# Optimization experiments

Measured on AMD Instinct MI355X. Metric: run time of the kernel, lower is better.

## Reference

```python
import jax, jax.numpy as jnp
import numpy as np

B, S, T, C, Q = 8, 4096, 2048, 256, 256  # batch, ctx_steps, q_steps, context_size, query_size


def setup_inputs() -> dict:
    key = jax.random.key(0)
    k1, k2, k3, k4 = jax.random.split(key, 4)
    context = jax.random.normal(k1, (B, S, C), dtype=jnp.float32)
    query = jax.random.normal(k2, (T, B, Q), dtype=jnp.float32)
    context_mask = jax.random.randint(k3, (B, S), 0, 2).astype(bool)  # True = masked
    W = jax.random.normal(k4, (C, Q), dtype=jnp.float32)  # bilinear weights [context_size, query_size]
    return {"context": context, "query": query, "context_mask": context_mask, "W": W}


def reference(context, query, context_mask, W):
    # temp = 'auto' -> sqrt(query_size)
    temp = jnp.asarray(np.sqrt(Q), dtype=context.dtype)
    # scores[b,t,s] = (context[b,s,:] @ W) . query[t,b,:]
    scores = jnp.einsum('bsc,cq,tbq->bts', context, W, query) / temp
    neg = jnp.finfo(scores.dtype).min
    scores = jnp.where(context_mask[:, None, :], neg, scores)  # mask over ctx_steps
    attn = jax.nn.softmax(scores, axis=2)  # [B, T, S]
    # rows whose entire context is masked -> attention zeroed
    all_masked = jnp.all(context_mask, axis=1)[:, None, None]
    attn = jnp.where(all_masked, jnp.zeros((), attn.dtype), attn)
    composition = jnp.einsum('bts,bsc->btc', attn, context)  # [B, T, C]
    # module returns (attn, composition) permuted to [T, B, ...]
    return attn.transpose(1, 0, 2), composition.transpose(1, 0, 2)
```

## Files before the change

### kernel.cpp

```cpp
#include <hip/hip_runtime.h>

#define B_ 8
#define S_ 4096
#define T_ 2048
#define C_ 256
#define Q_ 256
#define NROW (T_ * B_)

typedef _Float16 f16;
typedef _Float16 f16x8 __attribute__((ext_vector_type(8)));
typedef _Float16 f16x4 __attribute__((ext_vector_type(4)));
typedef float f32x4 __attribute__((ext_vector_type(4)));

#define MFMA(a, b, c) __builtin_amdgcn_mfma_f32_16x16x32_f16((a), (b), (c), 0, 0, 0)

__global__ void k_mask_mode(const unsigned char* __restrict__ mb, int* __restrict__ mode,
                            int* __restrict__ allm) {
  __shared__ int s0_, s123_;
  if (threadIdx.x == 0) { s0_ = 0; s123_ = 0; }
  __syncthreads();
  int a0 = 0, a123 = 0;
  int base = threadIdx.x * 128;
  for (int i = 0; i < 128; ++i) {
    int idx = base + i;
    int v = mb[idx];
    if (idx & 3) a123 |= v; else a0 |= v;
  }
  if (a0) atomicOr(&s0_, 1);
  if (a123) atomicOr(&s123_, 1);
  __syncthreads();
  if (threadIdx.x == 0) {
    int m;
    if (s123_ == 0 && s0_ == 0) m = 3;
    else if (s123_ == 0) m = 0;
    else if (s0_ == 0) m = 2;
    else m = 1;
    *mode = m;
  }
  if (threadIdx.x < B_) allm[threadIdx.x] = 1;
}

__global__ void k_expand_mask(const void* __restrict__ mp, const int* __restrict__ mode,
                              float* __restrict__ maskf, int* __restrict__ allm) {
  int i = blockIdx.x * 256 + threadIdx.x;
  int md = *mode;
  int m;
  if (md == 0)      m = ((const int*)mp)[i] != 0;
  else if (md == 1) m = ((const unsigned char*)mp)[i] != 0;
  else if (md == 2) m = ((const float*)mp)[i] != 0.0f;
  else              m = 0;
  maskf[i] = m ? 1.0f : 0.0f;
  if (!m) atomicAnd(&allm[i / S_], 0);
}

__global__ void k_conv_w(const float* __restrict__ W, f16* __restrict__ WT) {
  int i = blockIdx.x * 256 + threadIdx.x;
  int c = i >> 8, q = i & 255;
  WT[q * C_ + c] = (f16)W[i];
}

__global__ void k_conv_q(const float* __restrict__ q, f16* __restrict__ qT) {
  int i = blockIdx.x * 256 + threadIdx.x;
  int e = i * 4;
  int t = e / (B_ * Q_);
  int rb = e - t * (B_ * Q_);
  int b = rb >> 8;
  int qq = rb & 255;
  f32x4 v = *(const f32x4*)(q + e);
  f16x4 h; h[0] = (f16)v[0]; h[1] = (f16)v[1]; h[2] = (f16)v[2]; h[3] = (f16)v[3];
  *(f16x4*)(qT + ((size_t)(b * T_ + t)) * Q_ + qq) = h;
}

__global__ void k_transpose_ctx(const float* __restrict__ ctx, f16* __restrict__ ctxT) {
  __shared__ f16 tile[64][65];
  int s0 = blockIdx.x * 64, c0 = blockIdx.y * 64, b = blockIdx.z;
  int r = threadIdx.x >> 2;
  int cs = (threadIdx.x & 3) * 16;
  const float* src = ctx + ((size_t)(b * S_ + s0 + r)) * C_ + c0 + cs;
  f32x4 v0 = ((const f32x4*)src)[0];
  f32x4 v1 = ((const f32x4*)src)[1];
  f32x4 v2 = ((const f32x4*)src)[2];
  f32x4 v3 = ((const f32x4*)src)[3];
#pragma unroll
  for (int j = 0; j < 4; ++j) {
    tile[r][cs + j] = (f16)v0[j];
    tile[r][cs + 4 + j] = (f16)v1[j];
    tile[r][cs + 8 + j] = (f16)v2[j];
    tile[r][cs + 12 + j] = (f16)v3[j];
  }
  __syncthreads();
  int c = threadIdx.x >> 2;
  int ss = (threadIdx.x & 3) * 16;
  f16x8 o0, o1;
#pragma unroll
  for (int j = 0; j < 8; ++j) { o0[j] = tile[ss + j][c]; o1[j] = tile[ss + 8 + j][c]; }
  f16* dst = ctxT + ((size_t)(b * C_ + c0 + c)) * S_ + s0 + ss;
  *(f16x8*)dst = o0;
  *(f16x8*)(dst + 8) = o1;
}

__launch_bounds__(256, 2)
__global__ void k_gemm_cw(const float* __restrict__ ctx, const f16* __restrict__ WT,
                          f16* __restrict__ CW) {
  __shared__ alignas(16) f16 As[128 * 32];
  __shared__ alignas(16) f16 Bs[128 * 32];
  int n0 = blockIdx.x * 128;
  int m0 = blockIdx.y * 128;
  int tid = threadIdx.x;
  int w = tid >> 6, l = tid & 63;
  int wm = (w >> 1) * 64, wn = (w & 1) * 64;
  int lr = l & 15, lk = (l >> 4) * 8;
  f32x4 acc[4][4] = {};
  for (int k0 = 0; k0 < C_; k0 += 32) {
    __syncthreads();
#pragma unroll
    for (int it = 0; it < 2; ++it) {
      int h = (it * 256 + tid) * 8;
      int row = h >> 5, kk = h & 31;
      const float* ap = ctx + (size_t)(m0 + row) * C_ + k0 + kk;
      f32x4 x0 = ((const f32x4*)ap)[0];
      f32x4 x1 = ((const f32x4*)ap)[1];
      f16x8 hv;
#pragma unroll
      for (int j = 0; j < 4; ++j) { hv[j] = (f16)x0[j]; hv[4 + j] = (f16)x1[j]; }
      *(f16x8*)&As[row * 32 + kk] = hv;
    }
#pragma unroll
    for (int it = 0; it < 2; ++it) {
      int h = (it * 256 + tid) * 8;
      int row = h >> 5, kk = h & 31;
      *(f16x8*)&Bs[row * 32 + kk] = *(const f16x8*)&WT[(size_t)(n0 + row) * C_ + k0 + kk];
    }
    __syncthreads();
    f16x8 af[4], bf[4];
#pragma unroll
    for (int m = 0; m < 4; ++m) af[m] = *(const f16x8*)&As[(wm + m * 16 + lr) * 32 + lk];
#pragma unroll
    for (int n = 0; n < 4; ++n) bf[n] = *(const f16x8*)&Bs[(wn + n * 16 + lr) * 32 + lk];
#pragma unroll
    for (int m = 0; m < 4; ++m)
#pragma unroll
      for (int n = 0; n < 4; ++n) acc[m][n] = MFMA(af[m], bf[n], acc[m][n]);
  }
#pragma unroll
  for (int m = 0; m < 4; ++m)
#pragma unroll
    for (int n = 0; n < 4; ++n)
#pragma unroll
      for (int i = 0; i < 4; ++i) {
        int gm = m0 + wm + m * 16 + (l >> 4) * 4 + i;
        int gn = n0 + wn + n * 16 + lr;
        CW[(size_t)gm * Q_ + gn] = (f16)(acc[m][n][i] * 0.0625f);
      }
}

__launch_bounds__(256, 2)
__global__ void k_gemm_scores(const f16* __restrict__ qT, const f16* __restrict__ CW,
                              const float* __restrict__ maskf, float* __restrict__ attn,
                              float* __restrict__ pmax, float* __restrict__ psum) {
  __shared__ alignas(16) f16 As[128 * 32];
  __shared__ alignas(16) f16 Bs[128 * 32];
  int n0 = blockIdx.x * 128;
  int m0 = blockIdx.y * 128;
  int b = blockIdx.z;
  const f16* A = qT + (size_t)b * T_ * Q_;
  const f16* Bm = CW + (size_t)b * S_ * Q_;
  int tid = threadIdx.x;
  int w = tid >> 6, l = tid & 63;
  int wm = (w >> 1) * 64, wn = (w & 1) * 64;
  int lr = l & 15, lk = (l >> 4) * 8;
  f32x4 acc[4][4] = {};
  for (int k0 = 0; k0 < Q_; k0 += 32) {
    __syncthreads();
#pragma unroll
    for (int it = 0; it < 2; ++it) {
      int h = (it * 256 + tid) * 8;
      int row = h >> 5, kk = h & 31;
      *(f16x8*)&As[row * 32 + kk] = *(const f16x8*)&A[(size_t)(m0 + row) * Q_ + k0 + kk];
    }
#pragma unroll
    for (int it = 0; it < 2; ++it) {
      int h = (it * 256 + tid) * 8;
      int row = h >> 5, kk = h & 31;
      *(f16x8*)&Bs[row * 32 + kk] = *(const f16x8*)&Bm[(size_t)(n0 + row) * Q_ + k0 + kk];
    }
    __syncthreads();
    f16x8 af[4], bf[4];
#pragma unroll
    for (int m = 0; m < 4; ++m) af[m] = *(const f16x8*)&As[(wm + m * 16 + lr) * 32 + lk];
#pragma unroll
    for (int n = 0; n < 4; ++n) bf[n] = *(const f16x8*)&Bs[(wn + n * 16 + lr) * 32 + lk];
#pragma unroll
    for (int m = 0; m < 4; ++m)
#pragma unroll
      for (int n = 0; n < 4; ++n) acc[m][n] = MFMA(af[m], bf[n], acc[m][n]);
  }
  float msk[4];
#pragma unroll
  for (int n = 0; n < 4; ++n) msk[n] = maskf[b * S_ + n0 + wn + n * 16 + lr];
#pragma unroll
  for (int m = 0; m < 4; ++m)
#pragma unroll
    for (int n = 0; n < 4; ++n) {
      int gn = n0 + wn + n * 16 + lr;
#pragma unroll
      for (int i = 0; i < 4; ++i) {
        int gt = m0 + wm + m * 16 + (l >> 4) * 4 + i;
        float v = acc[m][n][i];
        if (msk[n] != 0.0f) v = -3.4e38f;
        acc[m][n][i] = v;
        attn[((size_t)gt * B_ + b) * S_ + gn] = v;
      }
    }
  int g = l >> 4;
  int ch = blockIdx.x * 2 + (w & 1);
#pragma unroll
  for (int m = 0; m < 4; ++m)
#pragma unroll
    for (int i = 0; i < 4; ++i) {
      float mx = fmaxf(fmaxf(acc[m][0][i], acc[m][1][i]), fmaxf(acc[m][2][i], acc[m][3][i]));
      mx = fmaxf(mx, __shfl_xor(mx, 1));
      mx = fmaxf(mx, __shfl_xor(mx, 2));
      mx = fmaxf(mx, __shfl_xor(mx, 4));
      mx = fmaxf(mx, __shfl_xor(mx, 8));
      float sm = 0.0f;
#pragma unroll
      for (int n = 0; n < 4; ++n) sm += __expf(acc[m][n][i] - mx);
      sm += __shfl_xor(sm, 1);
      sm += __shfl_xor(sm, 2);
      sm += __shfl_xor(sm, 4);
      sm += __shfl_xor(sm, 8);
      if (lr == 0) {
        int gt = m0 + wm + m * 16 + g * 4 + i;
        int r = gt * B_ + b;
        pmax[ch * NROW + r] = mx;
        psum[ch * NROW + r] = sm;
      }
    }
}

__global__ void k_finalize(const float* __restrict__ pmax, const float* __restrict__ psum,
                           float* __restrict__ rmax, float* __restrict__ rsum) {
  int r = blockIdx.x * 256 + threadIdx.x;
  float mx = -3.4e38f;
#pragma unroll 8
  for (int c = 0; c < 64; ++c) mx = fmaxf(mx, pmax[c * NROW + r]);
  float s = 0.0f;
#pragma unroll 8
  for (int c = 0; c < 64; ++c) s += psum[c * NROW + r] * __expf(pmax[c * NROW + r] - mx);
  rmax[r] = mx;
  rsum[r] = s;
}

__launch_bounds__(256, 2)
__global__ void k_comp(float* __restrict__ attn, const f16* __restrict__ ctxT,
                       const float* __restrict__ rmax, const float* __restrict__ rsum,
                       const int* __restrict__ allm, float* __restrict__ comp) {
  __shared__ alignas(16) f16 As[2][32 * 64];
  __shared__ alignas(16) f16 Bs[2][256 * 64];
  const int t0 = blockIdx.x * 32;
  const int b = blockIdx.y;
  const int tid = threadIdx.x;
  const int w = tid >> 6, l = tid & 63;
  const int lr = l & 15, hi = l >> 4;
  const int am = allm[b];
  const int ar = tid >> 4;
  const int cg = tid & 15;
  float mx0, mx1, inv0, inv1;
  float* aP0;
  float* aP1;
  {
    int r0 = (t0 + ar) * B_ + b;
    int r1 = (t0 + 16 + ar) * B_ + b;
    mx0 = rmax[r0]; mx1 = rmax[r1];
    inv0 = am ? 0.0f : (1.0f / rsum[r0]);
    inv1 = am ? 0.0f : (1.0f / rsum[r1]);
    aP0 = attn + (size_t)r0 * S_ + cg * 4;
    aP1 = attn + (size_t)r1 * S_ + cg * 4;
  }
  const int aswz = (cg * 8) ^ ((ar & 7) << 4);
  const int bc = tid >> 3;
  const int bs = tid & 7;
  const f16* bP = ctxT + ((size_t)(b * C_ + bc)) * S_ + bs * 8;
  const int bswz = (bs * 16) ^ ((bc & 7) << 4);
  f32x4 acc[2][4] = {};
  f32x4 aC0 = *(const f32x4*)aP0;
  f32x4 aC1 = *(const f32x4*)aP1;
  f16x8 bC[8];
#pragma unroll
  for (int i = 0; i < 8; ++i) bC[i] = *(const f16x8*)(bP + (size_t)i * 32 * S_);
  for (int k = 0; k < S_ / 64; ++k) {
    const int cur = k & 1;
    const int kn = (k + 1) * 64;
    f32x4 aN0 = *(const f32x4*)(aP0 + kn);
    f32x4 aN1 = *(const f32x4*)(aP1 + kn);
    f16x8 bN[8];
#pragma unroll
    for (int i = 0; i < 8; ++i) bN[i] = *(const f16x8*)(bP + (size_t)i * 32 * S_ + kn);
    f32x4 p0, p1;
#pragma unroll
    for (int e = 0; e < 4; ++e) {
      p0[e] = __expf(aC0[e] - mx0) * inv0;
      p1[e] = __expf(aC1[e] - mx1) * inv1;
    }
    *(f32x4*)(aP0 + k * 64) = p0;
    *(f32x4*)(aP1 + k * 64) = p1;
    f16x4 h0, h1;
#pragma unroll
    for (int e = 0; e < 4; ++e) { h0[e] = (f16)p0[e]; h1[e] = (f16)p1[e]; }
    *(f16x4*)((char*)As[cur] + ar * 128 + aswz) = h0;
    *(f16x4*)((char*)As[cur] + (16 + ar) * 128 + aswz) = h1;
#pragma unroll
    for (int i = 0; i < 8; ++i)
      *(f16x8*)((char*)Bs[cur] + (i * 32 + bc) * 128 + bswz) = bC[i];
    asm volatile("s_waitcnt lgkmcnt(0)" ::: "memory");
    __builtin_amdgcn_s_barrier();
    __builtin_amdgcn_sched_barrier(0);
#pragma unroll
    for (int kk = 0; kk < 2; ++kk) {
      const int cb = (kk * 64 + hi * 16) ^ ((lr & 7) << 4);
      f16x8 af[2], bf[4];
#pragma unroll
      for (int m = 0; m < 2; ++m)
        af[m] = *(const f16x8*)((char*)As[cur] + (m * 16 + lr) * 128 + cb);
#pragma unroll
      for (int n = 0; n < 4; ++n)
        bf[n] = *(const f16x8*)((char*)Bs[cur] + (w * 64 + n * 16 + lr) * 128 + cb);
#pragma unroll
      for (int m = 0; m < 2; ++m)
#pragma unroll
        for (int n = 0; n < 4; ++n) acc[m][n] = MFMA(af[m], bf[n], acc[m][n]);
    }
    aC0 = aN0; aC1 = aN1;
#pragma unroll
    for (int i = 0; i < 8; ++i) bC[i] = bN[i];
  }
#pragma unroll
  for (int m = 0; m < 2; ++m)
#pragma unroll
    for (int n = 0; n < 4; ++n)
#pragma unroll
      for (int i = 0; i < 4; ++i) {
        int tl = m * 16 + hi * 4 + i;
        int cc = w * 64 + n * 16 + lr;
        comp[((size_t)(t0 + tl) * B_ + b) * C_ + cc] = acc[m][n][i];
      }
}

extern "C" void kernel_launch(void* const* d_in, const int* in_sizes, int n_in,
                              void* d_out, int out_size, void* d_ws, size_t ws_size,
                              hipStream_t stream) {
  const float* ctx = (const float*)d_in[0];
  const float* query = (const float*)d_in[1];
  const void* mask = d_in[2];
  const float* W = (const float*)d_in[3];

  float* out = (float*)d_out;
  float* attn = out;
  float* comp = out + (size_t)T_ * B_ * S_;
  f16* CW = (f16*)comp;

  char* ws = (char*)d_ws;
  f16* ctxT = (f16*)(ws);
  f16* qT = (f16*)(ws + 16777216);
  f16* WT = (f16*)(ws + 25165824);
  float* maskf = (float*)(ws + 25296896);
  float* rmax = (float*)(ws + 25427968);
  float* rsum = (float*)(ws + 25493504);
  int* allm = (int*)(ws + 25559040);
  int* mode = (int*)(ws + 25559072);
  float* pmax = (float*)(ws + 25559168);
  float* psum = (float*)(ws + 29753472);

  k_mask_mode<<<1, 256, 0, stream>>>((const unsigned char*)mask, mode, allm);
  k_expand_mask<<<(B_ * S_) / 256, 256, 0, stream>>>(mask, mode, maskf, allm);
  k_conv_w<<<(C_ * Q_) / 256, 256, 0, stream>>>(W, WT);
  k_conv_q<<<(T_ * B_ * Q_ / 4) / 256, 256, 0, stream>>>(query, qT);
  k_transpose_ctx<<<dim3(S_ / 64, C_ / 64, B_), 256, 0, stream>>>(ctx, ctxT);
  k_gemm_cw<<<dim3(Q_ / 128, (B_ * S_) / 128), 256, 0, stream>>>(ctx, WT, CW);
  k_gemm_scores<<<dim3(S_ / 128, T_ / 128, B_), 256, 0, stream>>>(qT, CW, maskf, attn, pmax, psum);
  k_finalize<<<NROW / 256, 256, 0, stream>>>(pmax, psum, rmax, rsum);
  k_comp<<<dim3(T_ / 32, B_), 256, 0, stream>>>(attn, ctxT, rmax, rsum, allm, comp);
}
```

Before: 554.9 us.

## Recompute scores in fused softmax-composition kernel instead of round-tripping attn

Splits the scores pass into a stats-only GEMM that writes no attention matrix, then a fused kernel that recomputes scores per 64-column tile, normalizes with the final row max and sum, writes attn once, and feeds the fp16 probabilities straight from shared memory into the composition MFMA. This removes the first full write of the 268MB fp32 attn tensor and the k_comp pass that reads it back, at the cost of doing the QK GEMM twice. CW moves to a separate workspace region so comp is not aliased, and the old path is kept as a fallback when the workspace is too small.

Result: slower. 568.7 us (+2.5%).

```diff
diff --git a/kernel.cpp b/kernel.cpp
--- a/kernel.cpp
+++ b/kernel.cpp
@@ -210,6 +210,86 @@
         if (msk[n] != 0.0f) v = -3.4e38f;
         acc[m][n][i] = v;
         attn[((size_t)gt * B_ + b) * S_ + gn] = v;
+      }
+    }
+  int g = l >> 4;
+  int ch = blockIdx.x * 2 + (w & 1);
+#pragma unroll
+  for (int m = 0; m < 4; ++m)
+#pragma unroll
+    for (int i = 0; i < 4; ++i) {
+      float mx = fmaxf(fmaxf(acc[m][0][i], acc[m][1][i]), fmaxf(acc[m][2][i], acc[m][3][i]));
+      mx = fmaxf(mx, __shfl_xor(mx, 1));
+      mx = fmaxf(mx, __shfl_xor(mx, 2));
+      mx = fmaxf(mx, __shfl_xor(mx, 4));
+      mx = fmaxf(mx, __shfl_xor(mx, 8));
+      float sm = 0.0f;
+#pragma unroll
+      for (int n = 0; n < 4; ++n) sm += __expf(acc[m][n][i] - mx);
+      sm += __shfl_xor(sm, 1);
+      sm += __shfl_xor(sm, 2);
+      sm += __shfl_xor(sm, 4);
+      sm += __shfl_xor(sm, 8);
+      if (lr == 0) {
+        int gt = m0 + wm + m * 16 + g * 4 + i;
+        int r = gt * B_ + b;
+        pmax[ch * NROW + r] = mx;
+        psum[ch * NROW + r] = sm;
+      }
+    }
+}
+
+__launch_bounds__(256, 2)
+__global__ void k_gemm_stats(const f16* __restrict__ qT, const f16* __restrict__ CW,
+                             const float* __restrict__ maskf,
+                             float* __restrict__ pmax, float* __restrict__ psum) {
+  __shared__ alignas(16) f16 As[128 * 32];
+  __shared__ alignas(16) f16 Bs[128 * 32];
+  int n0 = blockIdx.x * 128;
+  int m0 = blockIdx.y * 128;
+  int b = blockIdx.z;
+  const f16* A = qT + (size_t)b * T_ * Q_;
+  const f16* Bm = CW + (size_t)b * S_ * Q_;
+  int tid = threadIdx.x;
+  int w = tid >> 6, l = tid & 63;
+  int wm = (w >> 1) * 64, wn = (w & 1) * 64;
+  int lr = l & 15, lk = (l >> 4) * 8;
+  f32x4 acc[4][4] = {};
+  for (int k0 = 0; k0 < Q_; k0 += 32) {
+    __syncthreads();
+#pragma unroll
+    for (int it = 0; it < 2; ++it) {
+      int h = (it * 256 + tid) * 8;
+      int row = h >> 5, kk = h & 31;
+      *(f16x8*)&As[row * 32 + kk] = *(const f16x8*)&A[(size_t)(m0 + row) * Q_ + k0 + kk];
+    }
+#pragma unroll
+    for (int it = 0; it < 2; ++it) {
+      int h = (it * 256 + tid) * 8;
+      int row = h >> 5, kk = h & 31;
+      *(f16x8*)&Bs[row * 32 + kk] = *(const f16x8*)&Bm[(size_t)(n0 + row) * Q_ + k0 + kk];
+    }
+    __syncthreads();
+    f16x8 af[4], bf[4];
+#pragma unroll
+    for (int m = 0; m < 4; ++m) af[m] = *(const f16x8*)&As[(wm + m * 16 + lr) * 32 + lk];
+#pragma unroll
+    for (int n = 0; n < 4; ++n) bf[n] = *(const f16x8*)&Bs[(wn + n * 16 + lr) * 32 + lk];
+#pragma unroll
+    for (int m = 0; m < 4; ++m)
+#pragma unroll
+      for (int n = 0; n < 4; ++n) acc[m][n] = MFMA(af[m], bf[n], acc[m][n]);
+  }
+  float msk[4];
+#pragma unroll
+  for (int n = 0; n < 4; ++n) msk[n] = maskf[b * S_ + n0 + wn + n * 16 + lr];
+#pragma unroll
+  for (int m = 0; m < 4; ++m)
+#pragma unroll
+    for (int n = 0; n < 4; ++n) {
+      if (msk[n] != 0.0f) {
+#pragma unroll
+        for (int i = 0; i < 4; ++i) acc[m][n][i] = -3.4e38f;
       }
     }
   int g = l >> 4;
@@ -347,6 +427,110 @@
       }
 }
 
+__launch_bounds__(256, 2)
+__global__ void k_fused(const f16* __restrict__ qT, const f16* __restrict__ CW,
+                        const f16* __restrict__ ctxT, const float* __restrict__ maskf,
+                        const float* __restrict__ rmax, const float* __restrict__ rsum,
+                        const int* __restrict__ allm,
+                        float* __restrict__ attn, float* __restrict__ comp) {
+  __shared__ alignas(16) f16 Bs[64 * 256];
+  __shared__ alignas(16) f16 Ps[32 * 64];
+  const int bid = blockIdx.x;
+  const int b = bid & 7, tc = bid >> 3;
+  const int t0 = tc * 32;
+  const int tid = threadIdx.x;
+  const int w = tid >> 6, l = tid & 63;
+  const int lr = l & 15, hi = l >> 4;
+  const int rswz = (lr & 7) << 4;
+  const int am = allm[b];
+  float smax[2][4], sinv[2][4];
+#pragma unroll
+  for (int m = 0; m < 2; ++m)
+#pragma unroll
+    for (int i = 0; i < 4; ++i) {
+      int r = (t0 + m * 16 + hi * 4 + i) * B_ + b;
+      smax[m][i] = rmax[r];
+      sinv[m][i] = am ? 0.0f : (1.0f / rsum[r]);
+    }
+  f16x8 af[2][8];
+#pragma unroll
+  for (int m = 0; m < 2; ++m)
+#pragma unroll
+    for (int kq = 0; kq < 8; ++kq)
+      af[m][kq] = *(const f16x8*)(qT + ((size_t)(b * T_ + t0 + m * 16 + lr)) * Q_ + kq * 32 + hi * 8);
+  const int brow = tid & 63;
+  const int bcolB = (tid >> 6) * 128;
+  const int bswz = (brow & 7) << 4;
+  const f16* cwBase = CW + (size_t)b * S_ * Q_;
+  {
+    const f16* src = cwBase + (size_t)brow * Q_ + bcolB / 2;
+#pragma unroll
+    for (int j = 0; j < 8; ++j)
+      *(f16x8*)((char*)Bs + ((brow * 512 + bcolB + j * 16) ^ bswz)) = *(const f16x8*)(src + j * 8);
+  }
+  float mk = maskf[b * S_ + w * 16 + lr];
+  f32x4 accC[2][4] = {};
+  __syncthreads();
+  for (int k = 0; k < S_ / 64; ++k) {
+    const int s0 = k * 64;
+    f32x4 accS[2] = {};
+#pragma unroll
+    for (int kq = 0; kq < 8; ++kq) {
+      f16x8 bfr = *(const f16x8*)((char*)Bs + (((w * 16 + lr) * 512 + kq * 64 + hi * 16) ^ rswz));
+#pragma unroll
+      for (int m = 0; m < 2; ++m) accS[m] = MFMA(af[m][kq], bfr, accS[m]);
+    }
+#pragma unroll
+    for (int m = 0; m < 2; ++m)
+#pragma unroll
+      for (int i = 0; i < 4; ++i) {
+        int tl = m * 16 + hi * 4 + i;
+        float p = (mk != 0.0f) ? 0.0f : __expf(accS[m][i] - smax[m][i]) * sinv[m][i];
+        attn[((size_t)(t0 + tl) * B_ + b) * S_ + s0 + w * 16 + lr] = p;
+        *(f16*)((char*)Ps + ((tl * 128 + (w * 16 + lr) * 2) ^ ((tl & 7) << 4))) = (f16)p;
+      }
+    __syncthreads();
+    f16x8 gB[8];
+    if (k < S_ / 64 - 1) {
+      const f16* src = cwBase + (size_t)(s0 + 64 + brow) * Q_ + bcolB / 2;
+#pragma unroll
+      for (int j = 0; j < 8; ++j) gB[j] = *(const f16x8*)(src + j * 8);
+    }
+    float mkn = (k < S_ / 64 - 1) ? maskf[b * S_ + s0 + 64 + w * 16 + lr] : 0.0f;
+#pragma unroll
+    for (int kk = 0; kk < 2; ++kk) {
+      f16x8 pa[2];
+#pragma unroll
+      for (int m = 0; m < 2; ++m)
+        pa[m] = *(const f16x8*)((char*)Ps + (((m * 16 + lr) * 128 + kk * 64 + hi * 16) ^ rswz));
+#pragma unroll
+      for (int n = 0; n < 4; ++n) {
+        f16x8 bc = *(const f16x8*)(ctxT + ((size_t)(b * C_ + w * 64 + n * 16 + lr)) * S_
+                                   + s0 + kk * 32 + hi * 8);
+#pragma unroll
+        for (int m = 0; m < 2; ++m) accC[m][n] = MFMA(pa[m], bc, accC[m][n]);
+      }
+    }
+    if (k < S_ / 64 - 1) {
+#pragma unroll
+      for (int j = 0; j < 8; ++j)
+        *(f16x8*)((char*)Bs + ((brow * 512 + bcolB + j * 16) ^ bswz)) = gB[j];
+    }
+    mk = mkn;
+    __syncthreads();
+  }
+#pragma unroll
+  for (int m = 0; m < 2; ++m)
+#pragma unroll
+    for (int n = 0; n < 4; ++n)
+#pragma unroll
+      for (int i = 0; i < 4; ++i) {
+        int tl = m * 16 + hi * 4 + i;
+        int cc = w * 64 + n * 16 + lr;
+        comp[((size_t)(t0 + tl) * B_ + b) * C_ + cc] = accC[m][n][i];
+      }
+}
+
 extern "C" void kernel_launch(void* const* d_in, const int* in_sizes, int n_in,
                               void* d_out, int out_size, void* d_ws, size_t ws_size,
                               hipStream_t stream) {
@@ -358,7 +542,6 @@
   float* out = (float*)d_out;
   float* attn = out;
   float* comp = out + (size_t)T_ * B_ * S_;
-  f16* CW = (f16*)comp;
 
   char* ws = (char*)d_ws;
   f16* ctxT = (f16*)(ws);
@@ -377,8 +560,19 @@
   k_conv_w<<<(C_ * Q_) / 256, 256, 0, stream>>>(W, WT);
   k_conv_q<<<(T_ * B_ * Q_ / 4) / 256, 256, 0, stream>>>(query, qT);
   k_transpose_ctx<<<dim3(S_ / 64, C_ / 64, B_), 256, 0, stream>>>(ctx, ctxT);
-  k_gemm_cw<<<dim3(Q_ / 128, (B_ * S_) / 128), 256, 0, stream>>>(ctx, WT, CW);
-  k_gemm_scores<<<dim3(S_ / 128, T_ / 128, B_), 256, 0, stream>>>(qT, CW, maskf, attn, pmax, psum);
-  k_finalize<<<NROW / 256, 256, 0, stream>>>(pmax, psum, rmax, rsum);
-  k_comp<<<dim3(T_ / 32, B_), 256, 0, stream>>>(attn, ctxT, rmax, rsum, allm, comp);
-}
+
+  if (ws_size >= (size_t)50724992) {
+    f16* CW2 = (f16*)(ws + 33947776);
+    k_gemm_cw<<<dim3(Q_ / 128, (B_ * S_) / 128), 256, 0, stream>>>(ctx, WT, CW2);
+    k_gemm_stats<<<dim3(S_ / 128, T_ / 128, B_), 256, 0, stream>>>(qT, CW2, maskf, pmax, psum);
+    k_finalize<<<NROW / 256, 256, 0, stream>>>(pmax, psum, rmax, rsum);
+    k_fused<<<dim3((T_ / 32) * B_), 256, 0, stream>>>(qT, CW2, ctxT, maskf, rmax, rsum, allm,
+                                                      attn, comp);
+  } else {
+    f16* CW = (f16*)comp;
+    k_gemm_cw<<<dim3(Q_ / 128, (B_ * S_) / 128), 256, 0, stream>>>(ctx, WT, CW);
+    k_gemm_scores<<<dim3(S_ / 128, T_ / 128, B_), 256, 0, stream>>>(qT, CW, maskf, attn, pmax, psum);
+    k_finalize<<<NROW / 256, 256, 0, stream>>>(pmax, psum, rmax, rsum);
+    k_comp<<<dim3(T_ / 32, B_), 256, 0, stream>>>(attn, ctxT, rmax, rsum, allm, comp);
+  }
+}
```
